# Performance work log

Measured on AMD Instinct MI355X. Metric: run time of the kernel, lower is better.

The kernel has to match this reference:

```python
import jax, jax.numpy as jnp
import numpy as np

N_NODES = 600_000
N_EDGES = 2_400_000
LEADS = 12
NUM_GRAPHS = N_NODES // LEADS  # 50_000
F_IN = 128
H = 64
OUT = 32


def setup_inputs() -> dict:
    key = jax.random.key(0)
    ks = jax.random.split(key, 12)
    x = jax.random.normal(ks[0], (N_NODES, F_IN), dtype=jnp.float32)
    src = jax.random.randint(ks[1], (N_EDGES,), 0, N_NODES)
    dst = jax.random.randint(ks[2], (N_EDGES,), 0, N_NODES)
    edge_index = jnp.stack([src, dst], axis=0)
    batch = jnp.repeat(jnp.arange(NUM_GRAPHS), LEADS)  # 12 nodes (leads) per graph
    s = 0.05
    W1 = jax.random.normal(ks[3], (F_IN, H), dtype=jnp.float32) * s
    b1 = jnp.zeros((H,), dtype=jnp.float32)
    W2 = jax.random.normal(ks[4], (H, H), dtype=jnp.float32) * s
    b2 = jnp.zeros((H,), dtype=jnp.float32)
    W3 = jax.random.normal(ks[5], (H, H), dtype=jnp.float32) * s
    b3 = jnp.zeros((H,), dtype=jnp.float32)
    Wa = jax.random.normal(ks[6], (H, H), dtype=jnp.float32) * s   # attention.attn (no bias)
    v = jax.random.normal(ks[7], (H, 1), dtype=jnp.float32) * s    # attention.v (no bias)
    Wl = jax.random.normal(ks[8], (2 * H, OUT), dtype=jnp.float32) * s  # self.lin
    bl = jnp.zeros((OUT,), dtype=jnp.float32)
    return {"x": x, "edge_index": edge_index, "batch": batch,
            "W1": W1, "b1": b1, "W2": W2, "b2": b2, "W3": W3, "b3": b3,
            "Wa": Wa, "v": v, "Wl": Wl, "bl": bl}


def reference(x, edge_index, batch, W1, b1, W2, b2, W3, b3, Wa, v, Wl, bl):
    n = x.shape[0]
    # GCNConv with self-loops and symmetric normalization (PyG defaults)
    loops = jnp.arange(n)
    row = jnp.concatenate([edge_index[0], loops])  # source
    col = jnp.concatenate([edge_index[1], loops])  # target
    deg = jax.ops.segment_sum(jnp.ones((row.shape[0],), dtype=x.dtype), col, num_segments=n)
    dinv = jnp.where(deg > 0, jax.lax.rsqrt(deg), 0.0)
    norm = dinv[row] * dinv[col]  # [E+N]

    def conv(h, W, b):
        h = h @ W  # transform first (small GEMM), then gather-scale-scatter
        agg = jax.ops.segment_sum(h[row] * norm[:, None], col, num_segments=n)
        return agg + b

    h = jax.nn.relu(conv(x, W1, b1))
    h = jax.nn.relu(conv(h, W2, b2))
    h = jax.nn.relu(conv(h, W3, b3))

    # lead attention over 12 consecutive nodes per graph
    h3 = h.reshape(-1, LEADS, H)               # [G, 12, 64]
    energy = jnp.tanh(h3 @ Wa)                 # [G, 12, 64]
    lweights = jax.nn.softmax(energy @ v, axis=1)  # [G, 12, 1]
    h = (h3 * lweights).reshape(-1, H)         # [N, 64]

    # global max pool + global mean pool per graph
    gmax = jax.ops.segment_max(h, batch, num_segments=NUM_GRAPHS)
    ssum = jax.ops.segment_sum(h, batch, num_segments=NUM_GRAPHS)
    cnt = jax.ops.segment_sum(jnp.ones((n,), dtype=h.dtype), batch, num_segments=NUM_GRAPHS)
    gmean = ssum / jnp.maximum(cnt, 1.0)[:, None]
    pooled = jnp.concatenate([gmax, gmean], axis=1)  # [G, 128]

    # dropout is identity in eval mode
    out = jax.nn.relu(pooled @ Wl + bl)  # [G, 32]
    return out, lweights
```

## Files before the change

### kernel.cpp

```cpp
#include <hip/hip_runtime.h>
#include <math.h>

#define N_NODES 600000
#define N_EDGES 2400000
#define HD 64
#define F_IN 128
#define LEADS 12
#define NUM_GRAPHS 50000
#define OUT_DIM 32
#define SCAN_BLOCKS 586

__global__ __launch_bounds__(256) void k_zero(int* __restrict__ cnt) {
    int i = blockIdx.x * 256 + threadIdx.x;
    if (i < N_NODES) cnt[i] = 0;
}

__global__ __launch_bounds__(256) void k_hist(const int* __restrict__ dst,
                                              int* __restrict__ cnt,
                                              int* __restrict__ rank) {
    int e = blockIdx.x * 256 + threadIdx.x;
    if (e < N_EDGES) rank[e] = atomicAdd(&cnt[dst[e]], 1);
}

__global__ __launch_bounds__(256) void k_scan1(const int* __restrict__ cnt,
                                               int* __restrict__ offs,
                                               int* __restrict__ bsum,
                                               float* __restrict__ dinv) {
    __shared__ int lds[256];
    int t = threadIdx.x;
    int base = blockIdx.x * 1024 + t * 4;
    int v[4];
#pragma unroll
    for (int j = 0; j < 4; ++j) v[j] = (base + j < N_NODES) ? cnt[base + j] : 0;
#pragma unroll
    for (int j = 0; j < 4; ++j)
        if (base + j < N_NODES) dinv[base + j] = rsqrtf((float)(v[j] + 1));
    int s = v[0] + v[1] + v[2] + v[3];
    lds[t] = s;
    __syncthreads();
    int val = s;
    for (int off = 1; off < 256; off <<= 1) {
        int other = (t >= off) ? lds[t - off] : 0;
        __syncthreads();
        val += other;
        lds[t] = val;
        __syncthreads();
    }
    if (t == 255) bsum[blockIdx.x] = val;
    int run = val - s;
#pragma unroll
    for (int j = 0; j < 4; ++j) {
        if (base + j < N_NODES) offs[base + j] = run;
        run += v[j];
    }
}

__global__ __launch_bounds__(256) void k_scan2(int* __restrict__ bsum) {
    __shared__ int lds[SCAN_BLOCKS];
    for (int i = threadIdx.x; i < SCAN_BLOCKS; i += 256) lds[i] = bsum[i];
    __syncthreads();
    if (threadIdx.x == 0) {
        int run = 0;
        for (int i = 0; i < SCAN_BLOCKS; ++i) {
            int c = lds[i];
            lds[i] = run;
            run += c;
        }
    }
    __syncthreads();
    for (int i = threadIdx.x; i < SCAN_BLOCKS; i += 256) bsum[i] = lds[i];
}

__global__ __launch_bounds__(256) void k_scan3(int* __restrict__ offs,
                                               const int* __restrict__ bsum) {
    int i = blockIdx.x * 256 + threadIdx.x;
    if (i < N_NODES) offs[i] += bsum[i >> 10];
}

__global__ __launch_bounds__(256) void k_fill(const int* __restrict__ src,
                                              const int* __restrict__ dst,
                                              const int* __restrict__ rank,
                                              const int* __restrict__ offs,
                                              int* __restrict__ eidx) {
    int e = blockIdx.x * 256 + threadIdx.x;
    if (e < N_EDGES) {
        int p = offs[dst[e]] + rank[e];
        eidx[p] = src[e];
    }
}

template <int K>
__global__ __launch_bounds__(256) void k_gemm(const float* __restrict__ in,
                                              const float* __restrict__ W,
                                              const float* __restrict__ dinv,
                                              float* __restrict__ tout) {
    __shared__ float lx[64 * (K + 1)];
    const int t = threadIdx.x;
    const int lane = t & 63;
    const int r0 = blockIdx.x * 64;

#pragma unroll
    for (int i = 0; i < K / 16; ++i) {
        int f = (t + i * 256) * 4;
        int r = f / K, k = f % K;
        float4 v = *(const float4*)(in + (size_t)(r0 + r) * K + k);
        float* p = &lx[r * (K + 1) + k];
        p[0] = v.x; p[1] = v.y; p[2] = v.z; p[3] = v.w;
    }
    __syncthreads();

    const int c0 = __builtin_amdgcn_readfirstlane((t >> 6) * 16);
    const float* Wp = W + c0;

    float acc[16];
#pragma unroll
    for (int cc = 0; cc < 16; ++cc) acc[cc] = 0.0f;

#pragma unroll
    for (int k = 0; k < K; ++k) {
        float xk = lx[lane * (K + 1) + k];
#pragma unroll
        for (int cc = 0; cc < 16; ++cc)
            acc[cc] = fmaf(xk, Wp[k * HD + cc], acc[cc]);
    }

    float di = dinv[r0 + lane];
#pragma unroll
    for (int cc = 0; cc < 16; ++cc) acc[cc] *= di;

    __syncthreads();
#pragma unroll
    for (int cc = 0; cc < 16; ++cc) lx[lane * 65 + c0 + cc] = acc[cc];
    __syncthreads();

    const int w = t >> 6;
#pragma unroll
    for (int i = 0; i < 16; ++i) {
        int r = i * 4 + w;
        tout[(size_t)(r0 + r) * HD + lane] = lx[r * 65 + lane];
    }
}

__global__ __launch_bounds__(256) void k_gather(const float* __restrict__ tp,
                                                const int* __restrict__ eidx,
                                                const int* __restrict__ offs,
                                                const int* __restrict__ cnt,
                                                const float* __restrict__ dinv,
                                                const float* __restrict__ bias,
                                                float* __restrict__ h) {
    const int wave = (blockIdx.x * 256 + threadIdx.x) >> 6;
    const int lane = threadIdx.x & 63;
    const int grp = lane >> 4, sl = lane & 15;
    const int node = wave * 4 + grp;

    const float4* tp4 = (const float4*)tp;
    float4 a0 = tp4[(size_t)node * 16 + sl];
    float4 a1 = {0.0f, 0.0f, 0.0f, 0.0f};

    const int start = offs[node];
    const int c = cnt[node];

    int cm = c;
#pragma unroll
    for (int off = 32; off >= 1; off >>= 1) cm = max(cm, __shfl_xor(cm, off));

    int j = 0;
    for (; j + 1 < cm; j += 2) {
        if (j < c) {
            int s0 = eidx[start + j];
            float4 v = tp4[(size_t)s0 * 16 + sl];
            a0.x += v.x; a0.y += v.y; a0.z += v.z; a0.w += v.w;
        }
        if (j + 1 < c) {
            int s1 = eidx[start + j + 1];
            float4 v = tp4[(size_t)s1 * 16 + sl];
            a1.x += v.x; a1.y += v.y; a1.z += v.z; a1.w += v.w;
        }
    }
    if (j < c) {
        int s0 = eidx[start + j];
        float4 v = tp4[(size_t)s0 * 16 + sl];
        a0.x += v.x; a0.y += v.y; a0.z += v.z; a0.w += v.w;
    }

    const float di = dinv[node];
    const float4 b4 = *(const float4*)(bias + sl * 4);
    float4 r;
    r.x = fmaxf(fmaf(di, a0.x + a1.x, b4.x), 0.0f);
    r.y = fmaxf(fmaf(di, a0.y + a1.y, b4.y), 0.0f);
    r.z = fmaxf(fmaf(di, a0.z + a1.z, b4.z), 0.0f);
    r.w = fmaxf(fmaf(di, a0.w + a1.w, b4.w), 0.0f);
    ((float4*)h)[(size_t)node * 16 + sl] = r;
}

__global__ __launch_bounds__(256) void k_attn(const float* __restrict__ h3,
                                              const float* __restrict__ Wa,
                                              const float* __restrict__ vvec,
                                              const float* __restrict__ Wl,
                                              const float* __restrict__ bl,
                                              float* __restrict__ out,
                                              float* __restrict__ lw) {
    __shared__ float lds_Wl[128 * 32];
    __shared__ float lds_h[4][LEADS * 64];
    __shared__ float lds_p[4][128];
    const int t = threadIdx.x;
    const int lane = t & 63;
    const int wid = t >> 6;

#pragma unroll
    for (int i = 0; i < 16; ++i) lds_Wl[t + i * 256] = Wl[t + i * 256];

    float wa[64];
#pragma unroll
    for (int k = 0; k < 64; ++k) wa[k] = Wa[k * 64 + lane];
    float vl = vvec[lane];
    __syncthreads();

    const int g = blockIdx.x * 4 + wid;

    float hv[LEADS];
#pragma unroll
    for (int r = 0; r < LEADS; ++r) {
        hv[r] = h3[(size_t)(g * LEADS + r) * 64 + lane];
        lds_h[wid][r * 64 + lane] = hv[r];
    }

    float s_[LEADS];
#pragma unroll
    for (int r = 0; r < LEADS; ++r) {
        float acc = 0.0f;
        const float4* h4 = (const float4*)&lds_h[wid][r * 64];
#pragma unroll
        for (int k4 = 0; k4 < 16; ++k4) {
            float4 hb = h4[k4];
            acc = fmaf(hb.x, wa[4 * k4 + 0], acc);
            acc = fmaf(hb.y, wa[4 * k4 + 1], acc);
            acc = fmaf(hb.z, wa[4 * k4 + 2], acc);
            acc = fmaf(hb.w, wa[4 * k4 + 3], acc);
        }
        float sc = tanhf(acc) * vl;
#pragma unroll
        for (int off = 32; off >= 1; off >>= 1) sc += __shfl_xor(sc, off);
        s_[r] = sc;
    }

    float m = s_[0];
#pragma unroll
    for (int r = 1; r < LEADS; ++r) m = fmaxf(m, s_[r]);
    float wgt[LEADS];
    float sum = 0.0f;
#pragma unroll
    for (int r = 0; r < LEADS; ++r) {
        wgt[r] = expf(s_[r] - m);
        sum += wgt[r];
    }
    float inv = 1.0f / sum;

    float tmp = wgt[0] * inv;
#pragma unroll
    for (int r = 1; r < LEADS; ++r) tmp = (lane == r) ? wgt[r] * inv : tmp;
    if (lane < LEADS) lw[g * LEADS + lane] = tmp;

    float gmax = -1e30f, gsum = 0.0f;
#pragma unroll
    for (int r = 0; r < LEADS; ++r) {
        float wh = hv[r] * (wgt[r] * inv);
        gmax = fmaxf(gmax, wh);
        gsum += wh;
    }
    lds_p[wid][lane] = gmax;
    lds_p[wid][64 + lane] = gsum * (1.0f / 12.0f);

    int o = lane & 31, half = lane >> 5;
    float acc2 = 0.0f;
#pragma unroll
    for (int k = 0; k < 64; ++k) {
        int kk = half * 64 + k;
        acc2 = fmaf(lds_p[wid][kk], lds_Wl[kk * 32 + o], acc2);
    }
    acc2 += __shfl_xor(acc2, 32);
    if (lane < 32) out[g * 32 + lane] = fmaxf(acc2 + bl[lane], 0.0f);
}

extern "C" void kernel_launch(void* const* d_in, const int* in_sizes, int n_in,
                              void* d_out, int out_size, void* d_ws, size_t ws_size,
                              hipStream_t stream) {
    const float* x  = (const float*)d_in[0];
    const int* ei   = (const int*)d_in[1];
    const int* src  = ei;
    const int* dst  = ei + N_EDGES;
    const float* W1 = (const float*)d_in[3];
    const float* b1 = (const float*)d_in[4];
    const float* W2 = (const float*)d_in[5];
    const float* b2 = (const float*)d_in[6];
    const float* W3 = (const float*)d_in[7];
    const float* b3 = (const float*)d_in[8];
    const float* Wa = (const float*)d_in[9];
    const float* vv = (const float*)d_in[10];
    const float* Wl = (const float*)d_in[11];
    const float* bl = (const float*)d_in[12];

    float* out = (float*)d_out;
    float* lw  = out + (size_t)NUM_GRAPHS * 32;

    float* dinv = (float*)d_ws;
    int* cnt    = (int*)(dinv + N_NODES);
    int* offs   = cnt + N_NODES;
    int* bsum   = offs + N_NODES;
    int* eidx   = bsum + 1024;
    float* T    = (float*)(eidx + N_EDGES);
    float* Hb   = T + (size_t)N_NODES * HD;
    int* rank   = (int*)T;

    const int gN = (N_NODES + 255) / 256;
    const int gE = (N_EDGES + 255) / 256;

    k_zero<<<gN, 256, 0, stream>>>(cnt);
    k_hist<<<gE, 256, 0, stream>>>(dst, cnt, rank);
    k_scan1<<<SCAN_BLOCKS, 256, 0, stream>>>(cnt, offs, bsum, dinv);
    k_scan2<<<1, 256, 0, stream>>>(bsum);
    k_scan3<<<gN, 256, 0, stream>>>(offs, bsum);
    k_fill<<<gE, 256, 0, stream>>>(src, dst, rank, offs, eidx);

    k_gemm<128><<<N_NODES / 64, 256, 0, stream>>>(x, W1, dinv, T);
    k_gather<<<N_NODES / 16, 256, 0, stream>>>(T, eidx, offs, cnt, dinv, b1, Hb);
    k_gemm<64><<<N_NODES / 64, 256, 0, stream>>>(Hb, W2, dinv, T);
    k_gather<<<N_NODES / 16, 256, 0, stream>>>(T, eidx, offs, cnt, dinv, b2, Hb);
    k_gemm<64><<<N_NODES / 64, 256, 0, stream>>>(Hb, W3, dinv, T);
    k_gather<<<N_NODES / 16, 256, 0, stream>>>(T, eidx, offs, cnt, dinv, b3, Hb);
    k_attn<<<NUM_GRAPHS / 4, 256, 0, stream>>>(Hb, Wa, vv, Wl, bl, out, lw);
}
```

Measured before the change: 1.459 ms.

## Fuse GCN neighbor gather with next layer's GEMM in one kernel

```diff
diff --git a/kernel.cpp b/kernel.cpp
--- a/kernel.cpp
+++ b/kernel.cpp
@@ -138,6 +138,98 @@
     for (int i = 0; i < 16; ++i) {
         int r = i * 4 + w;
         tout[(size_t)(r0 + r) * HD + lane] = lx[r * 65 + lane];
+    }
+}
+
+__global__ __launch_bounds__(256) void k_fused(const float* __restrict__ tp,
+                                               const int* __restrict__ eidx,
+                                               const int* __restrict__ offs,
+                                               const int* __restrict__ cnt,
+                                               const float* __restrict__ dinv,
+                                               const float* __restrict__ bias,
+                                               const float* __restrict__ W,
+                                               float* __restrict__ tout) {
+    __shared__ float lhx[64 * 65];
+    const int t = threadIdx.x;
+    const int lane = t & 63;
+    const int w = t >> 6;
+    const int r0 = blockIdx.x * 64;
+    const int grp = lane >> 4, sl = lane & 15;
+
+    const float4* tp4 = (const float4*)tp;
+    const float4 b4 = *(const float4*)(bias + sl * 4);
+
+#pragma unroll
+    for (int p = 0; p < 4; ++p) {
+        const int nl = p * 16 + w * 4 + grp;
+        const int node = r0 + nl;
+
+        float4 a0 = tp4[(size_t)node * 16 + sl];
+        float4 a1 = {0.0f, 0.0f, 0.0f, 0.0f};
+
+        const int start = offs[node];
+        const int c = cnt[node];
+
+        int cm = c;
+#pragma unroll
+        for (int off = 32; off >= 1; off >>= 1) cm = max(cm, __shfl_xor(cm, off));
+
+        int j = 0;
+        for (; j + 1 < cm; j += 2) {
+            if (j < c) {
+                int s0 = eidx[start + j];
+                float4 v = tp4[(size_t)s0 * 16 + sl];
+                a0.x += v.x; a0.y += v.y; a0.z += v.z; a0.w += v.w;
+            }
+            if (j + 1 < c) {
+                int s1 = eidx[start + j + 1];
+                float4 v = tp4[(size_t)s1 * 16 + sl];
+                a1.x += v.x; a1.y += v.y; a1.z += v.z; a1.w += v.w;
+            }
+        }
+        if (j < c) {
+            int s0 = eidx[start + j];
+            float4 v = tp4[(size_t)s0 * 16 + sl];
+            a0.x += v.x; a0.y += v.y; a0.z += v.z; a0.w += v.w;
+        }
+
+        const float di = dinv[node];
+        float* pl = &lhx[nl * 65 + sl * 4];
+        pl[0] = fmaxf(fmaf(di, a0.x + a1.x, b4.x), 0.0f);
+        pl[1] = fmaxf(fmaf(di, a0.y + a1.y, b4.y), 0.0f);
+        pl[2] = fmaxf(fmaf(di, a0.z + a1.z, b4.z), 0.0f);
+        pl[3] = fmaxf(fmaf(di, a0.w + a1.w, b4.w), 0.0f);
+    }
+    __syncthreads();
+
+    const int c0 = __builtin_amdgcn_readfirstlane(w * 16);
+    const float* Wp = W + c0;
+
+    float acc[16];
+#pragma unroll
+    for (int cc = 0; cc < 16; ++cc) acc[cc] = 0.0f;
+
+#pragma unroll
+    for (int k = 0; k < HD; ++k) {
+        float xk = lhx[lane * 65 + k];
+#pragma unroll
+        for (int cc = 0; cc < 16; ++cc)
+            acc[cc] = fmaf(xk, Wp[k * HD + cc], acc[cc]);
+    }
+
+    float di2 = dinv[r0 + lane];
+#pragma unroll
+    for (int cc = 0; cc < 16; ++cc) acc[cc] *= di2;
+
+    __syncthreads();
+#pragma unroll
+    for (int cc = 0; cc < 16; ++cc) lhx[lane * 65 + c0 + cc] = acc[cc];
+    __syncthreads();
+
+#pragma unroll
+    for (int i = 0; i < 16; ++i) {
+        int r = i * 4 + w;
+        tout[(size_t)(r0 + r) * HD + lane] = lhx[r * 65 + lane];
     }
 }
 
@@ -323,10 +415,8 @@
     k_fill<<<gE, 256, 0, stream>>>(src, dst, rank, offs, eidx);
 
     k_gemm<128><<<N_NODES / 64, 256, 0, stream>>>(x, W1, dinv, T);
-    k_gather<<<N_NODES / 16, 256, 0, stream>>>(T, eidx, offs, cnt, dinv, b1, Hb);
-    k_gemm<64><<<N_NODES / 64, 256, 0, stream>>>(Hb, W2, dinv, T);
-    k_gather<<<N_NODES / 16, 256, 0, stream>>>(T, eidx, offs, cnt, dinv, b2, Hb);
-    k_gemm<64><<<N_NODES / 64, 256, 0, stream>>>(Hb, W3, dinv, T);
+    k_fused<<<N_NODES / 64, 256, 0, stream>>>(T, eidx, offs, cnt, dinv, b1, W2, Hb);
+    k_fused<<<N_NODES / 64, 256, 0, stream>>>(Hb, eidx, offs, cnt, dinv, b2, W3, T);
     k_gather<<<N_NODES / 16, 256, 0, stream>>>(T, eidx, offs, cnt, dinv, b3, Hb);
     k_attn<<<NUM_GRAPHS / 4, 256, 0, stream>>>(Hb, Wa, vv, Wl, bl, out, lw);
 }
```

Result: no change. 1.438 ms (-1.4%).
